# Kernel tuning notes

Hardware: AMD Instinct MI355X
Metric: run time of the kernel (lower is better)

Reference implementation:

```python
import jax, jax.numpy as jnp
import numpy as np


def hard_sigmoid(x):
    # Keras hard_sigmoid: clip(0.2*x + 0.5, 0, 1)
    return jnp.clip(0.2 * x + 0.5, 0.0, 1.0)


def setup_inputs() -> dict:
    key = jax.random.key(0)
    k1, k2, k3 = jax.random.split(key, 3)
    B, H, W, C = 32, 64, 64, 256
    x = jax.random.normal(k1, (B, H, W, C), dtype=jnp.float32)
    # glorot_uniform over (C, W, H): fan_in = W (last-two matmul dims are W x H)
    limit = np.sqrt(6.0 / (W + H)).astype(np.float32)
    Wq = jax.random.uniform(k2, (C, W, H), minval=-limit, maxval=limit, dtype=jnp.float32)
    Wk = jax.random.uniform(k3, (C, W, H), minval=-limit, maxval=limit, dtype=jnp.float32)
    return {"x": x, "Wq": Wq, "Wk": Wk}


def reference(x, Wq, Wk):
    # x: [B, H, W, C] -> [B, C, H, W]
    xt = jnp.transpose(x, (0, 3, 1, 2))
    # projections: [B,C,H,W] @ [C,W,H] (broadcast over B) -> [B,C,H,H]
    q = hard_sigmoid(jnp.einsum('bchw,cwk->bchk', xt, Wq))
    K = jnp.tanh(jnp.einsum('bchw,cwk->bchk', xt, Wk))
    # scores: q @ K^T over last two dims -> [B,C,H,H]
    qk = hard_sigmoid(jnp.einsum('bchk,bcmk->bchm', q, K))
    qk = jax.nn.softmax(qk, axis=-1)
    # output: [B,C,H,W] @ [B,C,W(==H),H] -> [B,C,H,H]
    out = jnp.einsum('bchw,bcwm->bchm', xt, qk)
    # back to channels-last [B,H,W,C]
    return jnp.transpose(out, (0, 2, 3, 1))
```

## Files before the change

### kernel.cpp

```cpp
#include <hip/hip_runtime.h>


typedef short short8 __attribute__((ext_vector_type(8)));
typedef float floatx4 __attribute__((ext_vector_type(4)));
typedef unsigned int uint;

__device__ __forceinline__ uint cvtpk(float a, float b) {
  uint r;
  asm("v_cvt_pk_bf16_f32 %0, %1, %2" : "=v"(r) : "v"(a), "v"(b));
  return r;
}
__device__ __forceinline__ short8 u4s8(uint a, uint b, uint c, uint d) {
  union { uint u[4]; short8 s; } t;
  t.u[0] = a; t.u[1] = b; t.u[2] = c; t.u[3] = d;
  return t.s;
}
__device__ __forceinline__ float hsg(float x) {
  return fminf(fmaxf(0.2f * x + 0.5f, 0.f), 1.f);
}

__device__ __forceinline__ void pl32swap(uint A, uint C, uint& lo, uint& hi, int quad) {
#if __has_builtin(__builtin_amdgcn_permlane32_swap)
  auto r = __builtin_amdgcn_permlane32_swap(A, C, false, false);
  lo = (uint)r[0]; hi = (uint)r[1];
#else
  uint sA = __shfl_xor(A, 32), sC = __shfl_xor(C, 32);
  bool up = quad >= 2;
  lo = up ? sC : A;
  hi = up ? C : sA;
#endif
}
__device__ __forceinline__ void pl16swap(uint A, uint C, uint& lo, uint& hi, int quad) {
#if __has_builtin(__builtin_amdgcn_permlane16_swap)
  auto r = __builtin_amdgcn_permlane16_swap(A, C, false, false);
  lo = (uint)r[0]; hi = (uint)r[1];
#else
  uint sA = (uint)__builtin_amdgcn_ds_swizzle((int)A, 0x401F);
  uint sC = (uint)__builtin_amdgcn_ds_swizzle((int)C, 0x401F);
  bool odd = quad & 1;
  lo = odd ? sC : A;
  hi = odd ? C : sA;
#endif
}
__device__ __forceinline__ short8 xchg4(uint A, uint B, uint C, uint D, int quad) {
  uint Ap, Cp, Bp, Dp, t0, t1, t2, t3;
  pl32swap(A, C, Ap, Cp, quad);
  pl32swap(B, D, Bp, Dp, quad);
  pl16swap(Ap, Cp, t0, t2, quad);
  pl16swap(Bp, Dp, t1, t3, quad);
  return u4s8(t0, t1, t2, t3);
}

__global__ __launch_bounds__(256) void prep_w(const float* __restrict__ Wq,
                                              const float* __restrict__ Wk,
                                              unsigned short* __restrict__ ws) {
  __shared__ __align__(16) unsigned char sm[4 * 8704];
  const int tid = threadIdx.x, lane = tid & 63, wid = tid >> 6;
  const int task = blockIdx.x * 4 + wid;
  const int c = task & 255;
  const float* wp = ((task >> 8) ? Wk : Wq) + (size_t)c * 4096;
  unsigned char* buf = sm + wid * 8704;
  const int l15 = lane & 15, quad = lane >> 4;
#pragma unroll 4
  for (int j = 0; j < 16; ++j) {
    int f4 = j * 64 + lane;
    float4 v = *(const float4*)(wp + (size_t)f4 * 4);
    int w = f4 >> 4, k0 = (f4 & 15) << 2;
    uint2 pk; pk.x = cvtpk(v.x, v.y); pk.y = cvtpk(v.z, v.w);
    *(uint2*)(buf + w * 136 + k0 * 2) = pk;
  }
  unsigned short* dst = ws + (size_t)task * 4096;
#pragma unroll
  for (int kt = 0; kt < 4; ++kt)
#pragma unroll
    for (int ks = 0; ks < 2; ++ks) {
      const unsigned short* p = (const unsigned short*)buf + (ks * 32 + quad * 8) * 68 + (kt * 16 + l15);
      short8 af = u4s8((uint)p[0]   | ((uint)p[68]  << 16),
                       (uint)p[136] | ((uint)p[204] << 16),
                       (uint)p[272] | ((uint)p[340] << 16),
                       (uint)p[408] | ((uint)p[476] << 16));
      *(short8*)(dst + ((kt * 2 + ks) * 64 + lane) * 8) = af;
    }
}

__global__ __launch_bounds__(1024, 4) void fused_attn(
    const float* __restrict__ x, const unsigned short* __restrict__ wsp,
    float* __restrict__ out) {
  __shared__ __align__(16) unsigned char smem[16 * 8192];

  const int tid  = threadIdx.x;
  const int lane = tid & 63;
  const int wid  = tid >> 6;
  const int l15  = lane & 15;
  const int quad = lane >> 4;

  const int b    = blockIdx.x & 31;
  const int cg16 = blockIdx.x >> 5;
  const int c0   = cg16 << 4;
  const int c    = c0 + wid;

  unsigned char* buf0 = smem + wid * 8192;

  const short8* wqf = (const short8*)wsp + (size_t)c * 512;
  const short8* wkf = wqf + 256 * 512;

  short8 aq[4][2];
#pragma unroll
  for (int kt = 0; kt < 4; ++kt)
#pragma unroll
    for (int ks = 0; ks < 2; ++ks) aq[kt][ks] = wqf[(kt * 2 + ks) * 64 + lane];

  {
    const int ch4 = tid & 3, grp = tid >> 2;
    const float* xb = x + (size_t)b * 4096 * 256 + c0 + ch4 * 4;
#pragma unroll
    for (int bat = 0; bat < 2; ++bat) {
      float4 va[4], vb[4];
#pragma unroll
      for (int i = 0; i < 4; ++i) {
        int pair = (bat * 4 + i) * 256 + grp;
        int h = pair >> 5, w0 = (pair & 31) << 1;
        const float* src = xb + (size_t)(h * 64 + w0) * 256;
        va[i] = *(const float4*)src;
        vb[i] = *(const float4*)(src + 256);
      }
#pragma unroll
      for (int i = 0; i < 4; ++i) {
        int pair = (bat * 4 + i) * 256 + grp;
        int h = pair >> 5, w0 = (pair & 31) << 1;
        uint off = (uint)(h * 128 + (((w0 >> 3) ^ (h & 7)) << 4) + ((w0 & 7) << 1));
        unsigned char* base = smem + (size_t)(ch4 * 4) * 8192 + off;
        *(uint*)(base + 0 * 8192) = cvtpk(va[i].x, vb[i].x);
        *(uint*)(base + 1 * 8192) = cvtpk(va[i].y, vb[i].y);
        *(uint*)(base + 2 * 8192) = cvtpk(va[i].z, vb[i].z);
        *(uint*)(base + 3 * 8192) = cvtpk(va[i].w, vb[i].w);
      }
    }
  }
  __syncthreads();

  const floatx4 zero4 = {0.f, 0.f, 0.f, 0.f};
  floatx4 acc[16];

#pragma unroll
  for (int i = 0; i < 16; ++i) acc[i] = zero4;
#pragma unroll
  for (int ht = 0; ht < 4; ++ht) {
    int r = ht * 16 + l15;
    short8 x0 = *(const short8*)(buf0 + r * 128 + (((quad) ^ (r & 7)) << 4));
    short8 x1 = *(const short8*)(buf0 + r * 128 + (((4 + quad) ^ (r & 7)) << 4));
    __builtin_amdgcn_s_setprio(1);
#pragma unroll
    for (int kt = 0; kt < 4; ++kt) {
      acc[kt * 4 + ht] = __builtin_amdgcn_mfma_f32_16x16x32_bf16(aq[kt][0], x0, acc[kt * 4 + ht], 0, 0, 0);
      acc[kt * 4 + ht] = __builtin_amdgcn_mfma_f32_16x16x32_bf16(aq[kt][1], x1, acc[kt * 4 + ht], 0, 0, 0);
    }
    __builtin_amdgcn_s_setprio(0);
  }

  short8 qf[4][2];
#pragma unroll
  for (int ht = 0; ht < 4; ++ht) {
    uint s[4][2];
#pragma unroll
    for (int kt = 0; kt < 4; ++kt) {
      floatx4 a = acc[kt * 4 + ht];
      s[kt][0] = cvtpk(hsg(a[0]), hsg(a[1]));
      s[kt][1] = cvtpk(hsg(a[2]), hsg(a[3]));
    }
#pragma unroll
    for (int ks = 0; ks < 2; ++ks)
      qf[ht][ks] = xchg4(s[2 * ks][0], s[2 * ks][1], s[2 * ks + 1][0], s[2 * ks + 1][1], quad);
  }

#pragma unroll
  for (int i = 0; i < 16; ++i) acc[i] = zero4;
#pragma unroll
  for (int kt = 0; kt < 4; ++kt) {
    short8 a0 = wkf[(kt * 2 + 0) * 64 + lane];
    short8 a1 = wkf[(kt * 2 + 1) * 64 + lane];
    __builtin_amdgcn_s_setprio(1);
#pragma unroll
    for (int ht = 0; ht < 4; ++ht) {
      int r = ht * 16 + l15;
      short8 x0 = *(const short8*)(buf0 + r * 128 + (((quad) ^ (r & 7)) << 4));
      short8 x1 = *(const short8*)(buf0 + r * 128 + (((4 + quad) ^ (r & 7)) << 4));
      acc[kt * 4 + ht] = __builtin_amdgcn_mfma_f32_16x16x32_bf16(a0, x0, acc[kt * 4 + ht], 0, 0, 0);
      acc[kt * 4 + ht] = __builtin_amdgcn_mfma_f32_16x16x32_bf16(a1, x1, acc[kt * 4 + ht], 0, 0, 0);
    }
    __builtin_amdgcn_s_setprio(0);
  }
  short8 kf[4][2];
#pragma unroll
  for (int ht = 0; ht < 4; ++ht) {
    uint t[4][2];
#pragma unroll
    for (int kt = 0; kt < 4; ++kt) {
      floatx4 a = acc[kt * 4 + ht];
      float kv[4];
#pragma unroll
      for (int i = 0; i < 4; ++i) {
        float e = __expf(2.f * a[i]);
        kv[i] = 1.f - 2.f / (e + 1.f);
      }
      t[kt][0] = cvtpk(kv[0], kv[1]);
      t[kt][1] = cvtpk(kv[2], kv[3]);
    }
#pragma unroll
    for (int ks = 0; ks < 2; ++ks)
      kf[ht][ks] = xchg4(t[2 * ks][0], t[2 * ks][1], t[2 * ks + 1][0], t[2 * ks + 1][1], quad);
  }

  short8 sf[4][2];
#pragma unroll
  for (int ks2 = 0; ks2 < 2; ++ks2) {
    floatx4 a2[8];
#pragma unroll
    for (int i = 0; i < 8; ++i) a2[i] = zero4;
    __builtin_amdgcn_s_setprio(1);
#pragma unroll
    for (int mt = 0; mt < 4; ++mt)
#pragma unroll
      for (int wtl = 0; wtl < 2; ++wtl) {
        int wt = ks2 * 2 + wtl;
        a2[wtl * 4 + mt] = __builtin_amdgcn_mfma_f32_16x16x32_bf16(qf[wt][0], kf[mt][0], a2[wtl * 4 + mt], 0, 0, 0);
        a2[wtl * 4 + mt] = __builtin_amdgcn_mfma_f32_16x16x32_bf16(qf[wt][1], kf[mt][1], a2[wtl * 4 + mt], 0, 0, 0);
      }
    __builtin_amdgcn_s_setprio(0);
#pragma unroll
    for (int i = 0; i < 8; ++i)
#pragma unroll
      for (int j = 0; j < 4; ++j) a2[i][j] = __expf(hsg(a2[i][j]));
    float inv2[2][4];
#pragma unroll
    for (int wtl = 0; wtl < 2; ++wtl)
#pragma unroll
      for (int i = 0; i < 4; ++i) {
        float pp = a2[wtl * 4 + 0][i] + a2[wtl * 4 + 1][i] + a2[wtl * 4 + 2][i] + a2[wtl * 4 + 3][i];
        pp += __shfl_xor(pp, 1, 16);
        pp += __shfl_xor(pp, 2, 16);
        pp += __shfl_xor(pp, 4, 16);
        pp += __shfl_xor(pp, 8, 16);
        inv2[wtl][i] = 1.f / pp;
      }
#pragma unroll
    for (int mt = 0; mt < 4; ++mt) {
      uint s0 = cvtpk(a2[mt][0] * inv2[0][0], a2[mt][1] * inv2[0][1]);
      uint s1 = cvtpk(a2[mt][2] * inv2[0][2], a2[mt][3] * inv2[0][3]);
      uint s2 = cvtpk(a2[4 + mt][0] * inv2[1][0], a2[4 + mt][1] * inv2[1][1]);
      uint s3 = cvtpk(a2[4 + mt][2] * inv2[1][2], a2[4 + mt][3] * inv2[1][3]);
      sf[mt][ks2] = xchg4(s0, s1, s2, s3, quad);
    }
  }

#pragma unroll
  for (int i = 0; i < 16; ++i) acc[i] = zero4;
#pragma unroll
  for (int ht = 0; ht < 4; ++ht) {
    int r = ht * 16 + l15;
    short8 x0 = *(const short8*)(buf0 + r * 128 + (((quad) ^ (r & 7)) << 4));
    short8 x1 = *(const short8*)(buf0 + r * 128 + (((4 + quad) ^ (r & 7)) << 4));
    __builtin_amdgcn_s_setprio(1);
#pragma unroll
    for (int mt = 0; mt < 4; ++mt) {
      acc[mt * 4 + ht] = __builtin_amdgcn_mfma_f32_16x16x32_bf16(sf[mt][0], x0, acc[mt * 4 + ht], 0, 0, 0);
      acc[mt * 4 + ht] = __builtin_amdgcn_mfma_f32_16x16x32_bf16(sf[mt][1], x1, acc[mt * 4 + ht], 0, 0, 0);
    }
    __builtin_amdgcn_s_setprio(0);
  }
#pragma unroll
  for (int mt = 0; mt < 4; ++mt)
#pragma unroll
    for (int ht = 0; ht < 4; ++ht) {
      floatx4 a = acc[mt * 4 + ht];
      uint2 pk; pk.x = cvtpk(a[0], a[1]); pk.y = cvtpk(a[2], a[3]);
      int h = ht * 16 + l15;
      *(uint2*)(buf0 + h * 128 + ((((mt * 2 + (quad >> 1)) ^ (h & 7))) << 4) + ((quad & 1) << 3)) = pk;
    }
  __syncthreads();

  {
    const int ch4 = tid & 3, grp = tid >> 2;
    const size_t outbase = (size_t)b * 4096 * 256 + c0 + ch4 * 4;
#pragma unroll
    for (int rep = 0; rep < 4; ++rep) {
      int qidx = rep * 256 + grp;
      int h = qidx >> 4, mq = qidx & 15;
      uint loff = (uint)(h * 128 + ((((mq >> 1) ^ (h & 7))) << 4) + ((mq & 1) << 3));
      float vals[4][4];
#pragma unroll
      for (int j = 0; j < 4; ++j) {
        uint2 d = *(const uint2*)(smem + (size_t)(ch4 * 4 + j) * 8192 + loff);
        vals[j][0] = __uint_as_float(d.x << 16);
        vals[j][1] = __uint_as_float(d.x & 0xFFFF0000u);
        vals[j][2] = __uint_as_float(d.y << 16);
        vals[j][3] = __uint_as_float(d.y & 0xFFFF0000u);
      }
      float* op = out + outbase + (size_t)(h * 64 + mq * 4) * 256;
#pragma unroll
      for (int jj = 0; jj < 4; ++jj) {
        float4 v = {vals[0][jj], vals[1][jj], vals[2][jj], vals[3][jj]};
        *(float4*)(op + (size_t)jj * 256) = v;
      }
    }
  }
}

extern "C" void kernel_launch(void* const* d_in, const int* in_sizes, int n_in,
                              void* d_out, int out_size, void* d_ws, size_t ws_size,
                              hipStream_t stream) {
  const float* x  = (const float*)d_in[0];
  const float* Wq = (const float*)d_in[1];
  const float* Wk = (const float*)d_in[2];
  unsigned short* ws = (unsigned short*)d_ws;
  prep_w<<<dim3(128), dim3(256), 0, stream>>>(Wq, Wk, ws);
  fused_attn<<<dim3(512), dim3(1024), 0, stream>>>(x, ws, (float*)d_out);
}
```

Before: 285.0 us.

## Process two batches per block with prefetch of next batch's x tile

Each block now handles two batch entries for its 16-channel group, loading the second batch's x slice into LDS while the first batch's Q/K projections run. X fragments are held in registers, and a separate LDS region stages output per 16-row tile, so writes to global memory are interleaved with compute. LDS grows to 160 KB and the grid halves to 256 blocks, which cuts occupancy and parallelism in exchange for hiding global-load latency.

```diff
diff --git a/kernel.cpp b/kernel.cpp
--- a/kernel.cpp
+++ b/kernel.cpp
@@ -4,6 +4,11 @@
 typedef short short8 __attribute__((ext_vector_type(8)));
 typedef float floatx4 __attribute__((ext_vector_type(4)));
 typedef unsigned int uint;
+
+#define R1OFF 131072
+
+#define BAR() do { asm volatile("s_waitcnt lgkmcnt(0)" ::: "memory"); \
+    __builtin_amdgcn_s_barrier(); __builtin_amdgcn_sched_barrier(0); } while (0)
 
 __device__ __forceinline__ uint cvtpk(float a, float b) {
   uint r;
@@ -49,6 +54,45 @@
   pl16swap(Ap, Cp, t0, t2, quad);
   pl16swap(Bp, Dp, t1, t3, quad);
   return u4s8(t0, t1, t2, t3);
+}
+
+__device__ __forceinline__ void stage_issue(const float* xb, int grp, int bat,
+                                            float4* va, float4* vb) {
+#pragma unroll
+  for (int i = 0; i < 4; ++i) {
+    int pair = (bat * 4 + i) * 256 + grp;
+    int h = pair >> 5, w0 = (pair & 31) << 1;
+    const float* src = xb + (size_t)(h * 64 + w0) * 256;
+    va[i] = *(const float4*)src;
+    vb[i] = *(const float4*)(src + 256);
+  }
+}
+__device__ __forceinline__ void stage_commit(unsigned char* sm, int grp, int ch4,
+                                             int bat, const float4* va, const float4* vb) {
+#pragma unroll
+  for (int i = 0; i < 4; ++i) {
+    int pair = (bat * 4 + i) * 256 + grp;
+    int h = pair >> 5, w0 = (pair & 31) << 1;
+    uint off = (uint)(h * 128 + (((w0 >> 3) ^ (h & 7)) << 4) + ((w0 & 7) << 1));
+    uint pw[4] = {cvtpk(va[i].x, vb[i].x), cvtpk(va[i].y, vb[i].y),
+                  cvtpk(va[i].z, vb[i].z), cvtpk(va[i].w, vb[i].w)};
+#pragma unroll
+    for (int j = 0; j < 4; ++j) {
+      int ch = ch4 * 4 + j;
+      *(uint*)(sm + ch * 8192 + (off ^ (uint)((ch & 7) << 4))) = pw[j];
+    }
+  }
+}
+__device__ __forceinline__ void ld_xf(const unsigned char* buf0, int l15, int quad,
+                                      uint cx, short8 xf[4][2]) {
+#pragma unroll
+  for (int rt = 0; rt < 4; ++rt) {
+    int r = rt * 16 + l15;
+#pragma unroll
+    for (int ks = 0; ks < 2; ++ks)
+      xf[rt][ks] = *(const short8*)(buf0 + r * 128 +
+                     (((uint)(((ks * 4 + quad) ^ (r & 7))) << 4) ^ cx));
+  }
 }
 
 __global__ __launch_bounds__(256) void prep_w(const float* __restrict__ Wq,
@@ -83,225 +127,207 @@
     }
 }
 
-__global__ __launch_bounds__(1024, 4) void fused_attn(
+__global__ __launch_bounds__(1024) void fused_attn(
     const float* __restrict__ x, const unsigned short* __restrict__ wsp,
     float* __restrict__ out) {
-  __shared__ __align__(16) unsigned char smem[16 * 8192];
+  __shared__ __align__(16) unsigned char smem[163840];
 
   const int tid  = threadIdx.x;
   const int lane = tid & 63;
   const int wid  = tid >> 6;
   const int l15  = lane & 15;
   const int quad = lane >> 4;
-
-  const int b    = blockIdx.x & 31;
-  const int cg16 = blockIdx.x >> 5;
+  const int ch4  = tid & 3;
+  const int grp  = tid >> 2;
+
+  const int cg16 = blockIdx.x & 15;
+  const int bq   = blockIdx.x >> 4;
   const int c0   = cg16 << 4;
   const int c    = c0 + wid;
-
-  unsigned char* buf0 = smem + wid * 8192;
+  const uint cx  = (uint)((wid & 7) << 4);
+
+  unsigned char* xbuf = smem + wid * 8192;
 
   const short8* wqf = (const short8*)wsp + (size_t)c * 512;
   const short8* wkf = wqf + 256 * 512;
-
-  short8 aq[4][2];
-#pragma unroll
-  for (int kt = 0; kt < 4; ++kt)
-#pragma unroll
-    for (int ks = 0; ks < 2; ++ks) aq[kt][ks] = wqf[(kt * 2 + ks) * 64 + lane];
+  const floatx4 zero4 = {0.f, 0.f, 0.f, 0.f};
 
   {
-    const int ch4 = tid & 3, grp = tid >> 2;
-    const float* xb = x + (size_t)b * 4096 * 256 + c0 + ch4 * 4;
-#pragma unroll
-    for (int bat = 0; bat < 2; ++bat) {
-      float4 va[4], vb[4];
-#pragma unroll
-      for (int i = 0; i < 4; ++i) {
-        int pair = (bat * 4 + i) * 256 + grp;
-        int h = pair >> 5, w0 = (pair & 31) << 1;
-        const float* src = xb + (size_t)(h * 64 + w0) * 256;
-        va[i] = *(const float4*)src;
-        vb[i] = *(const float4*)(src + 256);
-      }
-#pragma unroll
-      for (int i = 0; i < 4; ++i) {
-        int pair = (bat * 4 + i) * 256 + grp;
-        int h = pair >> 5, w0 = (pair & 31) << 1;
-        uint off = (uint)(h * 128 + (((w0 >> 3) ^ (h & 7)) << 4) + ((w0 & 7) << 1));
-        unsigned char* base = smem + (size_t)(ch4 * 4) * 8192 + off;
-        *(uint*)(base + 0 * 8192) = cvtpk(va[i].x, vb[i].x);
-        *(uint*)(base + 1 * 8192) = cvtpk(va[i].y, vb[i].y);
-        *(uint*)(base + 2 * 8192) = cvtpk(va[i].z, vb[i].z);
-        *(uint*)(base + 3 * 8192) = cvtpk(va[i].w, vb[i].w);
-      }
-    }
-  }
-  __syncthreads();
-
-  const floatx4 zero4 = {0.f, 0.f, 0.f, 0.f};
-  floatx4 acc[16];
-
-#pragma unroll
-  for (int i = 0; i < 16; ++i) acc[i] = zero4;
-#pragma unroll
-  for (int ht = 0; ht < 4; ++ht) {
-    int r = ht * 16 + l15;
-    short8 x0 = *(const short8*)(buf0 + r * 128 + (((quad) ^ (r & 7)) << 4));
-    short8 x1 = *(const short8*)(buf0 + r * 128 + (((4 + quad) ^ (r & 7)) << 4));
-    __builtin_amdgcn_s_setprio(1);
-#pragma unroll
-    for (int kt = 0; kt < 4; ++kt) {
-      acc[kt * 4 + ht] = __builtin_amdgcn_mfma_f32_16x16x32_bf16(aq[kt][0], x0, acc[kt * 4 + ht], 0, 0, 0);
-      acc[kt * 4 + ht] = __builtin_amdgcn_mfma_f32_16x16x32_bf16(aq[kt][1], x1, acc[kt * 4 + ht], 0, 0, 0);
-    }
-    __builtin_amdgcn_s_setprio(0);
-  }
-
-  short8 qf[4][2];
-#pragma unroll
-  for (int ht = 0; ht < 4; ++ht) {
-    uint s[4][2];
-#pragma unroll
-    for (int kt = 0; kt < 4; ++kt) {
-      floatx4 a = acc[kt * 4 + ht];
-      s[kt][0] = cvtpk(hsg(a[0]), hsg(a[1]));
-      s[kt][1] = cvtpk(hsg(a[2]), hsg(a[3]));
-    }
-#pragma unroll
-    for (int ks = 0; ks < 2; ++ks)
-      qf[ht][ks] = xchg4(s[2 * ks][0], s[2 * ks][1], s[2 * ks + 1][0], s[2 * ks + 1][1], quad);
-  }
-
-#pragma unroll
-  for (int i = 0; i < 16; ++i) acc[i] = zero4;
-#pragma unroll
-  for (int kt = 0; kt < 4; ++kt) {
-    short8 a0 = wkf[(kt * 2 + 0) * 64 + lane];
-    short8 a1 = wkf[(kt * 2 + 1) * 64 + lane];
-    __builtin_amdgcn_s_setprio(1);
+    const float* xb = x + (size_t)(bq * 2) * 4096 * 256 + c0 + ch4 * 4;
+    float4 va[4], vb[4];
+    stage_issue(xb, grp, 0, va, vb);
+    stage_commit(smem, grp, ch4, 0, va, vb);
+    stage_issue(xb, grp, 1, va, vb);
+    stage_commit(smem, grp, ch4, 1, va, vb);
+  }
+  BAR();
+  short8 xf[4][2];
+  ld_xf(xbuf, l15, quad, cx, xf);
+  BAR();
+
+#pragma unroll
+  for (int it = 0; it < 2; ++it) {
+    const bool pre = (it == 0);
+    float4 va[4], vb[4];
+    const float* xbn = nullptr;
+    if (pre) {
+      xbn = x + (size_t)(bq * 2 + it + 1) * 4096 * 256 + c0 + ch4 * 4;
+      stage_issue(xbn, grp, 0, va, vb);
+    }
+
+    short8 wr[4][2];
+#pragma unroll
+    for (int kt = 0; kt < 4; ++kt)
+#pragma unroll
+      for (int ks = 0; ks < 2; ++ks) wr[kt][ks] = wqf[(kt * 2 + ks) * 64 + lane];
+
+    short8 qf[4][2];
 #pragma unroll
     for (int ht = 0; ht < 4; ++ht) {
-      int r = ht * 16 + l15;
-      short8 x0 = *(const short8*)(buf0 + r * 128 + (((quad) ^ (r & 7)) << 4));
-      short8 x1 = *(const short8*)(buf0 + r * 128 + (((4 + quad) ^ (r & 7)) << 4));
-      acc[kt * 4 + ht] = __builtin_amdgcn_mfma_f32_16x16x32_bf16(a0, x0, acc[kt * 4 + ht], 0, 0, 0);
-      acc[kt * 4 + ht] = __builtin_amdgcn_mfma_f32_16x16x32_bf16(a1, x1, acc[kt * 4 + ht], 0, 0, 0);
-    }
-    __builtin_amdgcn_s_setprio(0);
-  }
-  short8 kf[4][2];
-#pragma unroll
-  for (int ht = 0; ht < 4; ++ht) {
-    uint t[4][2];
-#pragma unroll
-    for (int kt = 0; kt < 4; ++kt) {
-      floatx4 a = acc[kt * 4 + ht];
-      float kv[4];
-#pragma unroll
-      for (int i = 0; i < 4; ++i) {
-        float e = __expf(2.f * a[i]);
-        kv[i] = 1.f - 2.f / (e + 1.f);
-      }
-      t[kt][0] = cvtpk(kv[0], kv[1]);
-      t[kt][1] = cvtpk(kv[2], kv[3]);
-    }
-#pragma unroll
-    for (int ks = 0; ks < 2; ++ks)
-      kf[ht][ks] = xchg4(t[2 * ks][0], t[2 * ks][1], t[2 * ks + 1][0], t[2 * ks + 1][1], quad);
-  }
-
-  short8 sf[4][2];
-#pragma unroll
-  for (int ks2 = 0; ks2 < 2; ++ks2) {
-    floatx4 a2[8];
-#pragma unroll
-    for (int i = 0; i < 8; ++i) a2[i] = zero4;
-    __builtin_amdgcn_s_setprio(1);
-#pragma unroll
-    for (int mt = 0; mt < 4; ++mt)
-#pragma unroll
-      for (int wtl = 0; wtl < 2; ++wtl) {
-        int wt = ks2 * 2 + wtl;
-        a2[wtl * 4 + mt] = __builtin_amdgcn_mfma_f32_16x16x32_bf16(qf[wt][0], kf[mt][0], a2[wtl * 4 + mt], 0, 0, 0);
-        a2[wtl * 4 + mt] = __builtin_amdgcn_mfma_f32_16x16x32_bf16(qf[wt][1], kf[mt][1], a2[wtl * 4 + mt], 0, 0, 0);
-      }
-    __builtin_amdgcn_s_setprio(0);
-#pragma unroll
-    for (int i = 0; i < 8; ++i)
-#pragma unroll
-      for (int j = 0; j < 4; ++j) a2[i][j] = __expf(hsg(a2[i][j]));
-    float inv2[2][4];
-#pragma unroll
-    for (int wtl = 0; wtl < 2; ++wtl)
-#pragma unroll
-      for (int i = 0; i < 4; ++i) {
-        float pp = a2[wtl * 4 + 0][i] + a2[wtl * 4 + 1][i] + a2[wtl * 4 + 2][i] + a2[wtl * 4 + 3][i];
-        pp += __shfl_xor(pp, 1, 16);
-        pp += __shfl_xor(pp, 2, 16);
-        pp += __shfl_xor(pp, 4, 16);
-        pp += __shfl_xor(pp, 8, 16);
-        inv2[wtl][i] = 1.f / pp;
-      }
-#pragma unroll
-    for (int mt = 0; mt < 4; ++mt) {
-      uint s0 = cvtpk(a2[mt][0] * inv2[0][0], a2[mt][1] * inv2[0][1]);
-      uint s1 = cvtpk(a2[mt][2] * inv2[0][2], a2[mt][3] * inv2[0][3]);
-      uint s2 = cvtpk(a2[4 + mt][0] * inv2[1][0], a2[4 + mt][1] * inv2[1][1]);
-      uint s3 = cvtpk(a2[4 + mt][2] * inv2[1][2], a2[4 + mt][3] * inv2[1][3]);
-      sf[mt][ks2] = xchg4(s0, s1, s2, s3, quad);
-    }
-  }
-
-#pragma unroll
-  for (int i = 0; i < 16; ++i) acc[i] = zero4;
-#pragma unroll
-  for (int ht = 0; ht < 4; ++ht) {
-    int r = ht * 16 + l15;
-    short8 x0 = *(const short8*)(buf0 + r * 128 + (((quad) ^ (r & 7)) << 4));
-    short8 x1 = *(const short8*)(buf0 + r * 128 + (((4 + quad) ^ (r & 7)) << 4));
-    __builtin_amdgcn_s_setprio(1);
-#pragma unroll
-    for (int mt = 0; mt < 4; ++mt) {
-      acc[mt * 4 + ht] = __builtin_amdgcn_mfma_f32_16x16x32_bf16(sf[mt][0], x0, acc[mt * 4 + ht], 0, 0, 0);
-      acc[mt * 4 + ht] = __builtin_amdgcn_mfma_f32_16x16x32_bf16(sf[mt][1], x1, acc[mt * 4 + ht], 0, 0, 0);
-    }
-    __builtin_amdgcn_s_setprio(0);
-  }
-#pragma unroll
-  for (int mt = 0; mt < 4; ++mt)
+      floatx4 a4[4];
+#pragma unroll
+      for (int i = 0; i < 4; ++i) a4[i] = zero4;
+      __builtin_amdgcn_s_setprio(1);
+#pragma unroll
+      for (int kt = 0; kt < 4; ++kt) {
+        a4[kt] = __builtin_amdgcn_mfma_f32_16x16x32_bf16(wr[kt][0], xf[ht][0], a4[kt], 0, 0, 0);
+        a4[kt] = __builtin_amdgcn_mfma_f32_16x16x32_bf16(wr[kt][1], xf[ht][1], a4[kt], 0, 0, 0);
+      }
+      __builtin_amdgcn_s_setprio(0);
+      uint s[4][2];
+#pragma unroll
+      for (int kt = 0; kt < 4; ++kt) {
+        s[kt][0] = cvtpk(hsg(a4[kt][0]), hsg(a4[kt][1]));
+        s[kt][1] = cvtpk(hsg(a4[kt][2]), hsg(a4[kt][3]));
+      }
+#pragma unroll
+      for (int ks = 0; ks < 2; ++ks)
+        qf[ht][ks] = xchg4(s[2 * ks][0], s[2 * ks][1], s[2 * ks + 1][0], s[2 * ks + 1][1], quad);
+      if (pre && ht == 0) stage_commit(smem, grp, ch4, 0, va, vb);
+      if (pre && ht == 1) stage_issue(xbn, grp, 1, va, vb);
+    }
+
+#pragma unroll
+    for (int kt = 0; kt < 4; ++kt)
+#pragma unroll
+      for (int ks = 0; ks < 2; ++ks) wr[kt][ks] = wkf[(kt * 2 + ks) * 64 + lane];
+    if (pre) stage_commit(smem, grp, ch4, 1, va, vb);
+
+    short8 kf[4][2];
 #pragma unroll
     for (int ht = 0; ht < 4; ++ht) {
-      floatx4 a = acc[mt * 4 + ht];
-      uint2 pk; pk.x = cvtpk(a[0], a[1]); pk.y = cvtpk(a[2], a[3]);
-      int h = ht * 16 + l15;
-      *(uint2*)(buf0 + h * 128 + ((((mt * 2 + (quad >> 1)) ^ (h & 7))) << 4) + ((quad & 1) << 3)) = pk;
-    }
-  __syncthreads();
-
-  {
-    const int ch4 = tid & 3, grp = tid >> 2;
-    const size_t outbase = (size_t)b * 4096 * 256 + c0 + ch4 * 4;
-#pragma unroll
-    for (int rep = 0; rep < 4; ++rep) {
-      int qidx = rep * 256 + grp;
-      int h = qidx >> 4, mq = qidx & 15;
-      uint loff = (uint)(h * 128 + ((((mq >> 1) ^ (h & 7))) << 4) + ((mq & 1) << 3));
-      float vals[4][4];
-#pragma unroll
-      for (int j = 0; j < 4; ++j) {
-        uint2 d = *(const uint2*)(smem + (size_t)(ch4 * 4 + j) * 8192 + loff);
-        vals[j][0] = __uint_as_float(d.x << 16);
-        vals[j][1] = __uint_as_float(d.x & 0xFFFF0000u);
-        vals[j][2] = __uint_as_float(d.y << 16);
-        vals[j][3] = __uint_as_float(d.y & 0xFFFF0000u);
-      }
-      float* op = out + outbase + (size_t)(h * 64 + mq * 4) * 256;
-#pragma unroll
-      for (int jj = 0; jj < 4; ++jj) {
-        float4 v = {vals[0][jj], vals[1][jj], vals[2][jj], vals[3][jj]};
-        *(float4*)(op + (size_t)jj * 256) = v;
-      }
+      floatx4 a4[4];
+#pragma unroll
+      for (int i = 0; i < 4; ++i) a4[i] = zero4;
+      __builtin_amdgcn_s_setprio(1);
+#pragma unroll
+      for (int kt = 0; kt < 4; ++kt) {
+        a4[kt] = __builtin_amdgcn_mfma_f32_16x16x32_bf16(wr[kt][0], xf[ht][0], a4[kt], 0, 0, 0);
+        a4[kt] = __builtin_amdgcn_mfma_f32_16x16x32_bf16(wr[kt][1], xf[ht][1], a4[kt], 0, 0, 0);
+      }
+      __builtin_amdgcn_s_setprio(0);
+      uint t[4][2];
+#pragma unroll
+      for (int kt = 0; kt < 4; ++kt) {
+        float kv[4];
+#pragma unroll
+        for (int i = 0; i < 4; ++i) {
+          float e = __expf(2.f * a4[kt][i]);
+          kv[i] = 1.f - 2.f / (e + 1.f);
+        }
+        t[kt][0] = cvtpk(kv[0], kv[1]);
+        t[kt][1] = cvtpk(kv[2], kv[3]);
+      }
+#pragma unroll
+      for (int ks = 0; ks < 2; ++ks)
+        kf[ht][ks] = xchg4(t[2 * ks][0], t[2 * ks][1], t[2 * ks + 1][0], t[2 * ks + 1][1], quad);
+    }
+
+    short8 sf[4][2];
+#pragma unroll
+    for (int ks2 = 0; ks2 < 2; ++ks2) {
+      floatx4 a2[8];
+#pragma unroll
+      for (int i = 0; i < 8; ++i) a2[i] = zero4;
+      __builtin_amdgcn_s_setprio(1);
+#pragma unroll
+      for (int mt = 0; mt < 4; ++mt)
+#pragma unroll
+        for (int wtl = 0; wtl < 2; ++wtl) {
+          int wt = ks2 * 2 + wtl;
+          a2[wtl * 4 + mt] = __builtin_amdgcn_mfma_f32_16x16x32_bf16(qf[wt][0], kf[mt][0], a2[wtl * 4 + mt], 0, 0, 0);
+          a2[wtl * 4 + mt] = __builtin_amdgcn_mfma_f32_16x16x32_bf16(qf[wt][1], kf[mt][1], a2[wtl * 4 + mt], 0, 0, 0);
+        }
+      __builtin_amdgcn_s_setprio(0);
+#pragma unroll
+      for (int i = 0; i < 8; ++i)
+#pragma unroll
+        for (int j = 0; j < 4; ++j) a2[i][j] = __expf(hsg(a2[i][j]));
+      float inv2[2][4];
+#pragma unroll
+      for (int wtl = 0; wtl < 2; ++wtl)
+#pragma unroll
+        for (int i = 0; i < 4; ++i) {
+          float pp = a2[wtl * 4 + 0][i] + a2[wtl * 4 + 1][i] + a2[wtl * 4 + 2][i] + a2[wtl * 4 + 3][i];
+          pp += __shfl_xor(pp, 1, 16);
+          pp += __shfl_xor(pp, 2, 16);
+          pp += __shfl_xor(pp, 4, 16);
+          pp += __shfl_xor(pp, 8, 16);
+          inv2[wtl][i] = 1.f / pp;
+        }
+#pragma unroll
+      for (int mt = 0; mt < 4; ++mt) {
+        uint s0 = cvtpk(a2[mt][0] * inv2[0][0], a2[mt][1] * inv2[0][1]);
+        uint s1 = cvtpk(a2[mt][2] * inv2[0][2], a2[mt][3] * inv2[0][3]);
+        uint s2 = cvtpk(a2[4 + mt][0] * inv2[1][0], a2[4 + mt][1] * inv2[1][1]);
+        uint s3 = cvtpk(a2[4 + mt][2] * inv2[1][2], a2[4 + mt][3] * inv2[1][3]);
+        sf[mt][ks2] = xchg4(s0, s1, s2, s3, quad);
+      }
+    }
+
+    const size_t outbase = (size_t)(bq * 2 + it) * 4096 * 256 + c0 + ch4 * 4;
+#pragma unroll
+    for (int ht = 0; ht < 4; ++ht) {
+      floatx4 a4[4];
+#pragma unroll
+      for (int i = 0; i < 4; ++i) a4[i] = zero4;
+      __builtin_amdgcn_s_setprio(1);
+#pragma unroll
+      for (int mt = 0; mt < 4; ++mt) {
+        a4[mt] = __builtin_amdgcn_mfma_f32_16x16x32_bf16(sf[mt][0], xf[ht][0], a4[mt], 0, 0, 0);
+        a4[mt] = __builtin_amdgcn_mfma_f32_16x16x32_bf16(sf[mt][1], xf[ht][1], a4[mt], 0, 0, 0);
+      }
+      __builtin_amdgcn_s_setprio(0);
+#pragma unroll
+      for (int mt = 0; mt < 4; ++mt) {
+        uint2 pk; pk.x = cvtpk(a4[mt][0], a4[mt][1]); pk.y = cvtpk(a4[mt][2], a4[mt][3]);
+        *(uint2*)(smem + R1OFF + wid * 2048 + l15 * 128 +
+                  ((uint)(((mt * 2 + (quad >> 1)) ^ (l15 & 7) ^ (wid & 7))) << 4) +
+                  ((quad & 1) << 3)) = pk;
+      }
+      BAR();
+      if (pre && ht == 3) ld_xf(xbuf, l15, quad, cx, xf);
+      {
+        int r = grp >> 4, mq = grp & 15;
+        float vals[4][4];
+#pragma unroll
+        for (int j = 0; j < 4; ++j) {
+          int ch = ch4 * 4 + j;
+          uint2 d = *(const uint2*)(smem + R1OFF + ch * 2048 + r * 128 +
+                      ((uint)(((mq >> 1) ^ (r & 7) ^ (ch & 7))) << 4) + ((mq & 1) << 3));
+          vals[j][0] = __uint_as_float(d.x << 16);
+          vals[j][1] = __uint_as_float(d.x & 0xFFFF0000u);
+          vals[j][2] = __uint_as_float(d.y << 16);
+          vals[j][3] = __uint_as_float(d.y & 0xFFFF0000u);
+        }
+        float* op = out + outbase + (size_t)((ht * 16 + r) * 64 + mq * 4) * 256;
+#pragma unroll
+        for (int jj = 0; jj < 4; ++jj) {
+          float4 v = {vals[0][jj], vals[1][jj], vals[2][jj], vals[3][jj]};
+          *(float4*)(op + (size_t)jj * 256) = v;
+        }
+      }
+      BAR();
     }
   }
 }
@@ -314,5 +340,5 @@
   const float* Wk = (const float*)d_in[2];
   unsigned short* ws = (unsigned short*)d_ws;
   prep_w<<<dim3(128), dim3(256), 0, stream>>>(Wq, Wk, ws);
-  fused_attn<<<dim3(512), dim3(1024), 0, stream>>>(x, ws, (float*)d_out);
-}
+  fused_attn<<<dim3(256), dim3(1024), 0, stream>>>(x, ws, (float*)d_out);
+}
```

Result: slower. 361.6 us (+26.9%).
